# Performance work log

Measured on AMD Instinct MI355X. Metric: run time of the kernel, lower is better.

Reference implementation:

```python
import jax, jax.numpy as jnp
import numpy as np

B, S, D, H = 2, 2048, 1024, 16
DK = D // H

def setup_inputs() -> dict:
    key = jax.random.key(0)
    ks = jax.random.split(key, 11)
    scale = 1.0 / np.sqrt(D)
    inp = {
        'q': jax.random.normal(ks[0], (B, S, D), jnp.float32),
        'k': jax.random.normal(ks[1], (B, S, D), jnp.float32),
        'v': jax.random.normal(ks[2], (B, S, D), jnp.float32),
        'Wq': jax.random.normal(ks[3], (D, D), jnp.float32) * scale,
        'bq': jnp.zeros((D,), jnp.float32),
        'Wk': jax.random.normal(ks[4], (D, D), jnp.float32) * scale,
        'bk': jnp.zeros((D,), jnp.float32),
        'Wv': jax.random.normal(ks[5], (D, D), jnp.float32) * scale,
        'bv': jnp.zeros((D,), jnp.float32),
        'Wo': jax.random.normal(ks[6], (D, D), jnp.float32) * scale,
        'bo': jnp.zeros((D,), jnp.float32),
    }
    return inp

def reference(q, k, v, Wq, bq, Wk, bk, Wv, bv, Wo, bo):
    # linear projections
    qp = q @ Wq + bq   # [B,S,D]
    kp = k @ Wk + bk
    vp = v @ Wv + bv
    # split heads -> [B,H,S,DK]
    qh = qp.reshape(B, S, H, DK).transpose(0, 2, 1, 3)
    kh = kp.reshape(B, S, H, DK).transpose(0, 2, 1, 3)
    vh = vp.reshape(B, S, H, DK).transpose(0, 2, 1, 3)
    scaled = jnp.einsum('bhqd,bhkd->bhqk', qh, kh) / jnp.sqrt(jnp.float32(DK))
    attn_score = jax.nn.softmax(scaled, axis=-1)  # [B,H,S,S]
    x = jnp.einsum('bhqk,bhkd->bhqd', attn_score, vh)
    # dropout is identity in eval mode
    out = x.transpose(0, 2, 1, 3).reshape(B, S, D)
    return (out @ Wo + bo, attn_score)
```

## Files before the change

### kernel.cpp

```cpp
#include <hip/hip_runtime.h>
#include <hip/hip_bf16.h>
#include <stdint.h>
#include <stddef.h>

typedef unsigned short u16;
typedef __attribute__((ext_vector_type(8))) short short8;
typedef __attribute__((ext_vector_type(4))) short bfx4;
typedef __attribute__((ext_vector_type(4))) float f32x4;
typedef __attribute__((ext_vector_type(4))) float f4;

constexpr int B_ = 2, S_ = 2048, D_ = 1024, H_ = 16;
constexpr size_t OUT_ELEMS = (size_t)B_ * S_ * D_;

__device__ __forceinline__ u16 f2bf(float f) {
    union { float f; unsigned u; } v; v.f = f;
    unsigned r = 0x7FFFu + ((v.u >> 16) & 1u);
    return (u16)((v.u + r) >> 16);
}

__device__ __forceinline__ void gload16(const void* g, void* l) {
    auto gg = reinterpret_cast<const __attribute__((address_space(1))) unsigned*>(
        reinterpret_cast<uintptr_t>(g));
    auto ll = reinterpret_cast<__attribute__((address_space(3))) unsigned*>(
        reinterpret_cast<uintptr_t>(l));
    __builtin_amdgcn_global_load_lds(gg, ll, 16, 0, 0);
}

__global__ __launch_bounds__(256) void wtrans_kernel(
    const float* __restrict__ W0, const float* __restrict__ W1,
    const float* __restrict__ W2, const float* __restrict__ W3,
    u16* __restrict__ T0, u16* __restrict__ T1, u16* __restrict__ T2, u16* __restrict__ T3)
{
    __shared__ __align__(16) u16 Ts[64][72];
    const float* W = blockIdx.z == 0 ? W0 : blockIdx.z == 1 ? W1 : blockIdx.z == 2 ? W2 : W3;
    u16*         T = blockIdx.z == 0 ? T0 : blockIdx.z == 1 ? T1 : blockIdx.z == 2 ? T2 : T3;
    const int t = threadIdx.x;
    const int r0 = blockIdx.y * 64, c0 = blockIdx.x * 64;
    const int row = t >> 2, qd = t & 3;

    const float* src = W + (size_t)(r0 + row) * 1024 + c0 + qd * 16;
    u16 tmp[16];
    #pragma unroll
    for (int j = 0; j < 16; j += 4) {
        f4 v = *(const f4*)(src + j);
        tmp[j] = f2bf(v[0]); tmp[j+1] = f2bf(v[1]); tmp[j+2] = f2bf(v[2]); tmp[j+3] = f2bf(v[3]);
    }
    #pragma unroll
    for (int j = 0; j < 16; j++) Ts[row][qd * 16 + j] = tmp[j];
    __syncthreads();
    short8 o0, o1;
    #pragma unroll
    for (int j = 0; j < 8; j++) { o0[j] = (short)Ts[qd*16 + j][row]; o1[j] = (short)Ts[qd*16 + 8 + j][row]; }
    u16* dst = T + (size_t)(c0 + row) * 1024 + r0 + qd * 16;
    *(short8*)dst = o0;
    *(short8*)(dst + 8) = o1;
}

__global__ __launch_bounds__(256) void vtrans_kernel(const u16* __restrict__ vp, u16* __restrict__ vt)
{
    __shared__ __align__(16) u16 Vs[64][72];
    const int t = threadIdx.x;
    const int s0 = blockIdx.x * 64;
    const int bh = blockIdx.y, b = bh >> 4, h = bh & 15;
    #pragma unroll
    for (int i = 0; i < 2; i++) {
        int c = t + 256 * i, row = c >> 3, ch = c & 7;
        *(short8*)(&Vs[row][ch * 8]) =
            *(const short8*)(vp + ((size_t)b * S_ + s0 + row) * D_ + h * 64 + ch * 8);
    }
    __syncthreads();
    #pragma unroll
    for (int i = 0; i < 2; i++) {
        int c = t + 256 * i, d = c >> 3, ch = c & 7;
        short8 o;
        #pragma unroll
        for (int j = 0; j < 8; j++) o[j] = (short)Vs[ch * 8 + j][d];
        *(short8*)(vt + ((size_t)bh * 64 + d) * S_ + s0 + ch * 8) = o;
    }
}

struct Stage { short8 h[2]; };

__device__ __forceinline__ void stage_load_f32(Stage& st, const float* Af, int row0, int K, int k0, int t) {
    const int row = t >> 1, half = t & 1;
    const float* p = Af + (size_t)(row0 + row) * K + k0 + half * 16;
    #pragma unroll
    for (int j = 0; j < 2; j++) {
        f4 v0 = *(const f4*)(p + j * 8);
        f4 v1 = *(const f4*)(p + j * 8 + 4);
        short8 hh;
        hh[0]=(short)f2bf(v0[0]); hh[1]=(short)f2bf(v0[1]); hh[2]=(short)f2bf(v0[2]); hh[3]=(short)f2bf(v0[3]);
        hh[4]=(short)f2bf(v1[0]); hh[5]=(short)f2bf(v1[1]); hh[6]=(short)f2bf(v1[2]); hh[7]=(short)f2bf(v1[3]);
        st.h[j] = hh;
    }
}

__device__ __forceinline__ void stage_store_f32(const Stage& st, u16* Ls, int t) {
    const int row = t >> 1, half = t & 1;
    #pragma unroll
    for (int j = 0; j < 2; j++) {
        int byteo = half * 32 + j * 16;
        *(short8*)((char*)Ls + row * 64 + (byteo ^ ((row & 3) << 4))) = st.h[j];
    }
}

template<int A_IS_F32, int OUT_IS_F32>
__global__ __launch_bounds__(256, 3)
void gemm_bt(const void* __restrict__ A0, const void* __restrict__ A1, const void* __restrict__ A2,
             const u16* __restrict__ Bt0, const u16* __restrict__ Bt1, const u16* __restrict__ Bt2,
             const float* __restrict__ bi0, const float* __restrict__ bi1, const float* __restrict__ bi2,
             void* __restrict__ C0, void* __restrict__ C1, void* __restrict__ C2,
             int M, int N, int K, float sc0, float sc1, float sc2)
{
    __shared__ __align__(16) u16 As[2][128 * 32];
    __shared__ __align__(16) u16 Bs[2][128 * 32];

    const int z = blockIdx.z;
    const void*  Aptr  = z == 0 ? A0  : z == 1 ? A1  : A2;
    const u16*   Bt    = z == 0 ? Bt0 : z == 1 ? Bt1 : Bt2;
    const float* bias  = z == 0 ? bi0 : z == 1 ? bi1 : bi2;
    void*        Cptr  = z == 0 ? C0  : z == 1 ? C1  : C2;
    const float  scale = z == 0 ? sc0 : z == 1 ? sc1 : sc2;

    const int t = threadIdx.x;
    const int w = t >> 6, l = t & 63, lr = l >> 4, lc = l & 15;
    const int wr = w >> 1, wc = w & 1;
    const int row0 = blockIdx.y * 128, col0 = blockIdx.x * 128;
    const int NI = K >> 5;

    auto issueT = [&](const u16* P, int r0_, int i, u16* dst) {
        #pragma unroll
        for (int j = 0; j < 2; j++) {
            int off = j * 256 + t;
            int row = off >> 2, ch = off & 3;
            const char* src = (const char*)P + (((size_t)(r0_ + row) * K + i * 32) << 1)
                              + ((ch ^ (row & 3)) << 4);
            gload16(src, (char*)dst + off * 16);
        }
    };

    f32x4 acc[4][4] = {};
    Stage sa;
    issueT(Bt, col0, 0, Bs[0]);
    if constexpr (A_IS_F32) {
        stage_load_f32(sa, (const float*)Aptr, row0, K, 0, t);
        stage_store_f32(sa, As[0], t);
        stage_load_f32(sa, (const float*)Aptr, row0, K, 32, t);
    } else {
        issueT((const u16*)Aptr, row0, 0, As[0]);
    }
    __syncthreads();

    for (int i = 0; i < NI; i++) {
        const int p = i & 1;
        if (i + 1 < NI) {
            issueT(Bt, col0, i + 1, Bs[p ^ 1]);
            if constexpr (A_IS_F32) {
                stage_store_f32(sa, As[p ^ 1], t);
                const int kn = (i + 2 < NI) ? (i + 2) * 32 : 0;
                stage_load_f32(sa, (const float*)Aptr, row0, K, kn, t);
            } else {
                issueT((const u16*)Aptr, row0, i + 1, As[p ^ 1]);
            }
        }

        short8 af[4], bf_[4];
        #pragma unroll
        for (int mm = 0; mm < 4; mm++) {
            int r = wr * 64 + mm * 16 + lc;
            af[mm] = *(const short8*)((const char*)As[p] + r * 64 + ((lr * 16) ^ ((r & 3) << 4)));
        }
        #pragma unroll
        for (int nn = 0; nn < 4; nn++) {
            int r = wc * 64 + nn * 16 + lc;
            bf_[nn] = *(const short8*)((const char*)Bs[p] + r * 64 + ((lr * 16) ^ ((r & 3) << 4)));
        }
        #pragma unroll
        for (int mm = 0; mm < 4; mm++)
            #pragma unroll
            for (int nn = 0; nn < 4; nn++)
                acc[mm][nn] = __builtin_amdgcn_mfma_f32_16x16x32_bf16(af[mm], bf_[nn], acc[mm][nn], 0, 0, 0);
        __syncthreads();
    }

    float bv[4];
    #pragma unroll
    for (int nn = 0; nn < 4; nn++) bv[nn] = bias[col0 + wc * 64 + nn * 16 + lc];

    #pragma unroll
    for (int mm = 0; mm < 4; mm++) {
        const int row = row0 + wr * 64 + mm * 16 + lr * 4;
        #pragma unroll
        for (int nn = 0; nn < 4; nn++) {
            const int col = col0 + wc * 64 + nn * 16 + lc;
            #pragma unroll
            for (int r = 0; r < 4; r++) {
                float vv = (acc[mm][nn][r] + bv[nn]) * scale;
                if constexpr (OUT_IS_F32) ((float*)Cptr)[(size_t)(row + r) * N + col] = vv;
                else                      ((u16*) Cptr)[(size_t)(row + r) * N + col] = f2bf(vv);
            }
        }
    }
}

__global__ __launch_bounds__(256, 4)
void attn_kernel(const u16* __restrict__ qp, const u16* __restrict__ kp,
                 const u16* __restrict__ vt, float* __restrict__ Pout,
                 u16* __restrict__ xout)
{
    __shared__ __align__(16) u16 Qs[64 * 64];
    __shared__ __align__(16) u16 Ks[2][64 * 64];
    __shared__ __align__(16) u16 Vts[2][64 * 64];

    const int t = threadIdx.x;
    const int w = t >> 6, l = t & 63, lr = l >> 4, lc = l & 15;
    const int bid = blockIdx.x;
    const int s = ((bid & 7) << 7) | (bid >> 3);
    const int q0 = (s & 31) * 64;
    const int bh = s >> 5, b = bh >> 4, h = bh & 15;
    const float L2E = 1.4426950408889634f;
    constexpr int NT = S_ / 64;

    auto issueK = [&](int kt, int buf) {
        #pragma unroll
        for (int i = 0; i < 2; i++) {
            int off = i * 256 + t, row = off >> 3, ch = off & 7;
            const char* src = (const char*)kp + ((((size_t)b * S_ + kt * 64 + row) * D_ + h * 64) << 1)
                              + ((ch ^ (row & 7)) << 4);
            gload16(src, (char*)Ks[buf] + off * 16);
        }
    };
    auto issueV = [&](int kt, int buf) {
        #pragma unroll
        for (int i = 0; i < 2; i++) {
            int off = i * 256 + t, row = off >> 3, ch = off & 7;
            const char* src = (const char*)vt + ((((size_t)bh * 64 + row) * S_ + kt * 64) << 1)
                              + ((ch ^ (row & 7)) << 4);
            gload16(src, (char*)Vts[buf] + off * 16);
        }
    };

    issueK(0, 0);
    #pragma unroll
    for (int i = 0; i < 2; i++) {
        int c = t + 256 * i, row = c >> 3, ch = c & 7;
        short8 vq = *(const short8*)(qp + ((size_t)b * S_ + q0 + row) * D_ + h * 64 + ch * 8);
        *(short8*)((char*)Qs + row * 128 + ((ch * 16) ^ ((row & 7) << 4))) = vq;
    }
    __syncthreads();

    short8 qf[2];
    {
        int r = w * 16 + lc, sw = (r & 7) << 4;
        const char* qb = (const char*)Qs + r * 128;
        qf[0] = *(const short8*)(qb + ((lr * 16) ^ sw));
        qf[1] = *(const short8*)(qb + ((64 + lr * 16) ^ sw));
    }

    float sum = 0.f;
    for (int kt = 0; kt < NT; kt++) {
        const int p = kt & 1;
        if (kt + 1 < NT) issueK(kt + 1, p ^ 1);
        const char* Kb = (const char*)Ks[p];
        #pragma unroll
        for (int f = 0; f < 4; f++) {
            int r = f * 16 + lc, sw = (r & 7) << 4;
            const char* kb = Kb + r * 128;
            short8 k0 = *(const short8*)(kb + ((lr * 16) ^ sw));
            short8 k1 = *(const short8*)(kb + ((64 + lr * 16) ^ sw));
            f32x4 sacc = {};
            sacc = __builtin_amdgcn_mfma_f32_16x16x32_bf16(k0, qf[0], sacc, 0, 0, 0);
            sacc = __builtin_amdgcn_mfma_f32_16x16x32_bf16(k1, qf[1], sacc, 0, 0, 0);
            sum += exp2f(sacc[0] * L2E) + exp2f(sacc[1] * L2E)
                 + exp2f(sacc[2] * L2E) + exp2f(sacc[3] * L2E);
        }
        __syncthreads();
    }
    sum += __shfl_xor(sum, 16);
    sum += __shfl_xor(sum, 32);
    const float inv = 1.0f / sum;

    f32x4 xacc[4] = {};
    float* pbase = Pout + ((size_t)bh * S_ + q0 + w * 16 + lc) * S_ + lr * 4;

    issueK(0, 0); issueV(0, 0);
    __syncthreads();
    for (int kt = 0; kt < NT; kt++) {
        const int p = kt & 1;
        if (kt + 1 < NT) { issueK(kt + 1, p ^ 1); issueV(kt + 1, p ^ 1); }
        const char* Kb = (const char*)Ks[p];
        const char* Vb = (const char*)Vts[p];

        #pragma unroll
        for (int kk = 0; kk < 2; kk++) {
            union { unsigned u[4]; short8 s8; } pu;
            #pragma unroll
            for (int fo = 0; fo < 2; fo++) {
                const int f = kk * 2 + fo;
                int r = f * 16 + lc, sw = (r & 7) << 4;
                const char* kb = Kb + r * 128;
                short8 k0 = *(const short8*)(kb + ((lr * 16) ^ sw));
                short8 k1 = *(const short8*)(kb + ((64 + lr * 16) ^ sw));
                f32x4 sacc = {};
                sacc = __builtin_amdgcn_mfma_f32_16x16x32_bf16(k0, qf[0], sacc, 0, 0, 0);
                sacc = __builtin_amdgcn_mfma_f32_16x16x32_bf16(k1, qf[1], sacc, 0, 0, 0);
                f32x4 pv_;
                pv_[0] = exp2f(sacc[0] * L2E) * inv;
                pv_[1] = exp2f(sacc[1] * L2E) * inv;
                pv_[2] = exp2f(sacc[2] * L2E) * inv;
                pv_[3] = exp2f(sacc[3] * L2E) * inv;
                *(f32x4*)(pbase + (size_t)kt * 64 + f * 16) = pv_;
                pu.u[fo * 2 + 0] = (unsigned)f2bf(pv_[0]) | ((unsigned)f2bf(pv_[1]) << 16);
                pu.u[fo * 2 + 1] = (unsigned)f2bf(pv_[2]) | ((unsigned)f2bf(pv_[3]) << 16);
            }
            const short8 pa = pu.s8;
            #pragma unroll
            for (int n = 0; n < 4; n++) {
                int rr = n * 16 + lc, sw2 = (rr & 7) << 4;
                const char* vrow = Vb + rr * 128;
                union { bfx4 h[2]; short8 s8; } vu;
                vu.h[0] = *(const bfx4*)(vrow + ((kk * 64 + lr * 8) ^ sw2));
                vu.h[1] = *(const bfx4*)(vrow + ((kk * 64 + 32 + lr * 8) ^ sw2));
                xacc[n] = __builtin_amdgcn_mfma_f32_16x16x32_bf16(pa, vu.s8, xacc[n], 0, 0, 0);
            }
        }
        __syncthreads();
    }

    #pragma unroll
    for (int n = 0; n < 4; n++) {
        #pragma unroll
        for (int r = 0; r < 4; r++) {
            int row = q0 + w * 16 + lr * 4 + r;
            int col = h * 64 + n * 16 + lc;
            xout[((size_t)b * S_ + row) * D_ + col] = f2bf(xacc[n][r]);
        }
    }
}

extern "C" void kernel_launch(void* const* d_in, const int* in_sizes, int n_in,
                              void* d_out, int out_size, void* d_ws, size_t ws_size,
                              hipStream_t stream)
{
    const float* qin = (const float*)d_in[0];
    const float* kin = (const float*)d_in[1];
    const float* vin = (const float*)d_in[2];
    const float* Wq  = (const float*)d_in[3];
    const float* bq  = (const float*)d_in[4];
    const float* Wk  = (const float*)d_in[5];
    const float* bk  = (const float*)d_in[6];
    const float* Wv  = (const float*)d_in[7];
    const float* bv  = (const float*)d_in[8];
    const float* Wo  = (const float*)d_in[9];
    const float* bo  = (const float*)d_in[10];

    u16* base = (u16*)d_ws;
    u16* Wqt = base;
    u16* Wkt = base + 1048576;
    u16* Wvt = base + 2097152;
    u16* Wot = base + 3145728;
    u16* qpb = base + 4194304;
    u16* kpb = base + 8388608;
    u16* vpb = base + 12582912;
    u16* vtb = base + 16777216;
    u16* xb  = base + 20971520;

    float* out  = (float*)d_out;
    float* Pout = out + OUT_ELEMS;

    const int M = B_ * S_;

    wtrans_kernel<<<dim3(16, 16, 4), 256, 0, stream>>>(Wq, Wk, Wv, Wo, Wqt, Wkt, Wvt, Wot);
    gemm_bt<1, 0><<<dim3(8, 32, 3), 256, 0, stream>>>(
        qin, kin, vin, Wqt, Wkt, Wvt, bq, bk, bv, qpb, kpb, vpb, M, D_, D_, 0.125f, 1.0f, 1.0f);
    vtrans_kernel<<<dim3(32, 32), 256, 0, stream>>>(vpb, vtb);
    attn_kernel<<<1024, 256, 0, stream>>>(qpb, kpb, vtb, Pout, xb);
    gemm_bt<0, 1><<<dim3(8, 32, 1), 256, 0, stream>>>(
        xb, xb, xb, Wot, Wot, Wot, bo, bo, bo, out, out, out, M, D_, D_, 1.0f, 1.0f, 1.0f);
}
```

Measured before the change: 295.9 us.

## Precast inputs to bf16, remap GEMM tiles by XCD, drop LDS in attention

```diff
diff --git a/kernel.cpp b/kernel.cpp
--- a/kernel.cpp
+++ b/kernel.cpp
@@ -26,6 +26,21 @@
     __builtin_amdgcn_global_load_lds(gg, ll, 16, 0, 0);
 }
 
+__global__ __launch_bounds__(256) void cast_kernel(
+    const float* __restrict__ q, const float* __restrict__ k, const float* __restrict__ v,
+    u16* __restrict__ qo, u16* __restrict__ ko, u16* __restrict__ vo)
+{
+    const float* src = blockIdx.z == 0 ? q : blockIdx.z == 1 ? k : v;
+    u16*         dst = blockIdx.z == 0 ? qo : blockIdx.z == 1 ? ko : vo;
+    size_t i = ((size_t)blockIdx.x * 256 + threadIdx.x) * 8;
+    f4 a = *(const f4*)(src + i);
+    f4 b = *(const f4*)(src + i + 4);
+    short8 o;
+    o[0]=(short)f2bf(a[0]); o[1]=(short)f2bf(a[1]); o[2]=(short)f2bf(a[2]); o[3]=(short)f2bf(a[3]);
+    o[4]=(short)f2bf(b[0]); o[5]=(short)f2bf(b[1]); o[6]=(short)f2bf(b[2]); o[7]=(short)f2bf(b[3]);
+    *(short8*)(dst + i) = o;
+}
+
 __global__ __launch_bounds__(256) void wtrans_kernel(
     const float* __restrict__ W0, const float* __restrict__ W1,
     const float* __restrict__ W2, const float* __restrict__ W3,
@@ -79,34 +94,9 @@
     }
 }
 
-struct Stage { short8 h[2]; };
-
-__device__ __forceinline__ void stage_load_f32(Stage& st, const float* Af, int row0, int K, int k0, int t) {
-    const int row = t >> 1, half = t & 1;
-    const float* p = Af + (size_t)(row0 + row) * K + k0 + half * 16;
-    #pragma unroll
-    for (int j = 0; j < 2; j++) {
-        f4 v0 = *(const f4*)(p + j * 8);
-        f4 v1 = *(const f4*)(p + j * 8 + 4);
-        short8 hh;
-        hh[0]=(short)f2bf(v0[0]); hh[1]=(short)f2bf(v0[1]); hh[2]=(short)f2bf(v0[2]); hh[3]=(short)f2bf(v0[3]);
-        hh[4]=(short)f2bf(v1[0]); hh[5]=(short)f2bf(v1[1]); hh[6]=(short)f2bf(v1[2]); hh[7]=(short)f2bf(v1[3]);
-        st.h[j] = hh;
-    }
-}
-
-__device__ __forceinline__ void stage_store_f32(const Stage& st, u16* Ls, int t) {
-    const int row = t >> 1, half = t & 1;
-    #pragma unroll
-    for (int j = 0; j < 2; j++) {
-        int byteo = half * 32 + j * 16;
-        *(short8*)((char*)Ls + row * 64 + (byteo ^ ((row & 3) << 4))) = st.h[j];
-    }
-}
-
-template<int A_IS_F32, int OUT_IS_F32>
+template<int OUT_IS_F32>
 __global__ __launch_bounds__(256, 3)
-void gemm_bt(const void* __restrict__ A0, const void* __restrict__ A1, const void* __restrict__ A2,
+void gemm_bt(const u16* __restrict__ A0, const u16* __restrict__ A1, const u16* __restrict__ A2,
              const u16* __restrict__ Bt0, const u16* __restrict__ Bt1, const u16* __restrict__ Bt2,
              const float* __restrict__ bi0, const float* __restrict__ bi1, const float* __restrict__ bi2,
              void* __restrict__ C0, void* __restrict__ C1, void* __restrict__ C2,
@@ -116,7 +106,7 @@
     __shared__ __align__(16) u16 Bs[2][128 * 32];
 
     const int z = blockIdx.z;
-    const void*  Aptr  = z == 0 ? A0  : z == 1 ? A1  : A2;
+    const u16*   Aptr  = z == 0 ? A0  : z == 1 ? A1  : A2;
     const u16*   Bt    = z == 0 ? Bt0 : z == 1 ? Bt1 : Bt2;
     const float* bias  = z == 0 ? bi0 : z == 1 ? bi1 : bi2;
     void*        Cptr  = z == 0 ? C0  : z == 1 ? C1  : C2;
@@ -125,7 +115,10 @@
     const int t = threadIdx.x;
     const int w = t >> 6, l = t & 63, lr = l >> 4, lc = l & 15;
     const int wr = w >> 1, wc = w & 1;
-    const int row0 = blockIdx.y * 128, col0 = blockIdx.x * 128;
+    const int id = blockIdx.y * 8 + blockIdx.x;
+    const int xcd = id & 7, i_ = id >> 3;
+    const int row0 = ((xcd << 2) | ((i_ >> 4) << 1) | ((i_ >> 3) & 1)) * 128;
+    const int col0 = (i_ & 7) * 128;
     const int NI = K >> 5;
 
     auto issueT = [&](const u16* P, int r0_, int i, u16* dst) {
@@ -140,28 +133,15 @@
     };
 
     f32x4 acc[4][4] = {};
-    Stage sa;
     issueT(Bt, col0, 0, Bs[0]);
-    if constexpr (A_IS_F32) {
-        stage_load_f32(sa, (const float*)Aptr, row0, K, 0, t);
-        stage_store_f32(sa, As[0], t);
-        stage_load_f32(sa, (const float*)Aptr, row0, K, 32, t);
-    } else {
-        issueT((const u16*)Aptr, row0, 0, As[0]);
-    }
+    issueT(Aptr, row0, 0, As[0]);
     __syncthreads();
 
     for (int i = 0; i < NI; i++) {
         const int p = i & 1;
         if (i + 1 < NI) {
             issueT(Bt, col0, i + 1, Bs[p ^ 1]);
-            if constexpr (A_IS_F32) {
-                stage_store_f32(sa, As[p ^ 1], t);
-                const int kn = (i + 2 < NI) ? (i + 2) * 32 : 0;
-                stage_load_f32(sa, (const float*)Aptr, row0, K, kn, t);
-            } else {
-                issueT((const u16*)Aptr, row0, i + 1, As[p ^ 1]);
-            }
+            issueT(Aptr, row0, i + 1, As[p ^ 1]);
         }
 
         short8 af[4], bf_[4];
@@ -208,10 +188,6 @@
                  const u16* __restrict__ vt, float* __restrict__ Pout,
                  u16* __restrict__ xout)
 {
-    __shared__ __align__(16) u16 Qs[64 * 64];
-    __shared__ __align__(16) u16 Ks[2][64 * 64];
-    __shared__ __align__(16) u16 Vts[2][64 * 64];
-
     const int t = threadIdx.x;
     const int w = t >> 6, l = t & 63, lr = l >> 4, lc = l & 15;
     const int bid = blockIdx.x;
@@ -219,62 +195,25 @@
     const int q0 = (s & 31) * 64;
     const int bh = s >> 5, b = bh >> 4, h = bh & 15;
     const float L2E = 1.4426950408889634f;
-    constexpr int NT = S_ / 64;
-
-    auto issueK = [&](int kt, int buf) {
-        #pragma unroll
-        for (int i = 0; i < 2; i++) {
-            int off = i * 256 + t, row = off >> 3, ch = off & 7;
-            const char* src = (const char*)kp + ((((size_t)b * S_ + kt * 64 + row) * D_ + h * 64) << 1)
-                              + ((ch ^ (row & 7)) << 4);
-            gload16(src, (char*)Ks[buf] + off * 16);
-        }
-    };
-    auto issueV = [&](int kt, int buf) {
-        #pragma unroll
-        for (int i = 0; i < 2; i++) {
-            int off = i * 256 + t, row = off >> 3, ch = off & 7;
-            const char* src = (const char*)vt + ((((size_t)bh * 64 + row) * S_ + kt * 64) << 1)
-                              + ((ch ^ (row & 7)) << 4);
-            gload16(src, (char*)Vts[buf] + off * 16);
-        }
-    };
-
-    issueK(0, 0);
-    #pragma unroll
-    for (int i = 0; i < 2; i++) {
-        int c = t + 256 * i, row = c >> 3, ch = c & 7;
-        short8 vq = *(const short8*)(qp + ((size_t)b * S_ + q0 + row) * D_ + h * 64 + ch * 8);
-        *(short8*)((char*)Qs + row * 128 + ((ch * 16) ^ ((row & 7) << 4))) = vq;
-    }
-    __syncthreads();
-
-    short8 qf[2];
-    {
-        int r = w * 16 + lc, sw = (r & 7) << 4;
-        const char* qb = (const char*)Qs + r * 128;
-        qf[0] = *(const short8*)(qb + ((lr * 16) ^ sw));
-        qf[1] = *(const short8*)(qb + ((64 + lr * 16) ^ sw));
-    }
+
+    const u16* qrow = qp + ((size_t)b * S_ + q0 + w * 16 + lc) * D_ + h * 64;
+    const short8 qf0 = *(const short8*)(qrow + lr * 8);
+    const short8 qf1 = *(const short8*)(qrow + 32 + lr * 8);
+
+    const u16* kbase = kp + (size_t)b * S_ * D_ + h * 64;
+    const u16* vbase = vt + (size_t)bh * 64 * S_;
 
     float sum = 0.f;
-    for (int kt = 0; kt < NT; kt++) {
-        const int p = kt & 1;
-        if (kt + 1 < NT) issueK(kt + 1, p ^ 1);
-        const char* Kb = (const char*)Ks[p];
-        #pragma unroll
-        for (int f = 0; f < 4; f++) {
-            int r = f * 16 + lc, sw = (r & 7) << 4;
-            const char* kb = Kb + r * 128;
-            short8 k0 = *(const short8*)(kb + ((lr * 16) ^ sw));
-            short8 k1 = *(const short8*)(kb + ((64 + lr * 16) ^ sw));
-            f32x4 sacc = {};
-            sacc = __builtin_amdgcn_mfma_f32_16x16x32_bf16(k0, qf[0], sacc, 0, 0, 0);
-            sacc = __builtin_amdgcn_mfma_f32_16x16x32_bf16(k1, qf[1], sacc, 0, 0, 0);
-            sum += exp2f(sacc[0] * L2E) + exp2f(sacc[1] * L2E)
-                 + exp2f(sacc[2] * L2E) + exp2f(sacc[3] * L2E);
-        }
-        __syncthreads();
+    #pragma unroll 2
+    for (int kg = 0; kg < S_ / 16; kg++) {
+        const u16* krow = kbase + (size_t)(kg * 16 + lc) * D_;
+        short8 k0 = *(const short8*)(krow + lr * 8);
+        short8 k1 = *(const short8*)(krow + 32 + lr * 8);
+        f32x4 sacc = {};
+        sacc = __builtin_amdgcn_mfma_f32_16x16x32_bf16(k0, qf0, sacc, 0, 0, 0);
+        sacc = __builtin_amdgcn_mfma_f32_16x16x32_bf16(k1, qf1, sacc, 0, 0, 0);
+        sum += exp2f(sacc[0] * L2E) + exp2f(sacc[1] * L2E)
+             + exp2f(sacc[2] * L2E) + exp2f(sacc[3] * L2E);
     }
     sum += __shfl_xor(sum, 16);
     sum += __shfl_xor(sum, 32);
@@ -283,48 +222,33 @@
     f32x4 xacc[4] = {};
     float* pbase = Pout + ((size_t)bh * S_ + q0 + w * 16 + lc) * S_ + lr * 4;
 
-    issueK(0, 0); issueV(0, 0);
-    __syncthreads();
-    for (int kt = 0; kt < NT; kt++) {
-        const int p = kt & 1;
-        if (kt + 1 < NT) { issueK(kt + 1, p ^ 1); issueV(kt + 1, p ^ 1); }
-        const char* Kb = (const char*)Ks[p];
-        const char* Vb = (const char*)Vts[p];
-
-        #pragma unroll
-        for (int kk = 0; kk < 2; kk++) {
-            union { unsigned u[4]; short8 s8; } pu;
-            #pragma unroll
-            for (int fo = 0; fo < 2; fo++) {
-                const int f = kk * 2 + fo;
-                int r = f * 16 + lc, sw = (r & 7) << 4;
-                const char* kb = Kb + r * 128;
-                short8 k0 = *(const short8*)(kb + ((lr * 16) ^ sw));
-                short8 k1 = *(const short8*)(kb + ((64 + lr * 16) ^ sw));
-                f32x4 sacc = {};
-                sacc = __builtin_amdgcn_mfma_f32_16x16x32_bf16(k0, qf[0], sacc, 0, 0, 0);
-                sacc = __builtin_amdgcn_mfma_f32_16x16x32_bf16(k1, qf[1], sacc, 0, 0, 0);
-                f32x4 pv_;
-                pv_[0] = exp2f(sacc[0] * L2E) * inv;
-                pv_[1] = exp2f(sacc[1] * L2E) * inv;
-                pv_[2] = exp2f(sacc[2] * L2E) * inv;
-                pv_[3] = exp2f(sacc[3] * L2E) * inv;
-                *(f32x4*)(pbase + (size_t)kt * 64 + f * 16) = pv_;
-                pu.u[fo * 2 + 0] = (unsigned)f2bf(pv_[0]) | ((unsigned)f2bf(pv_[1]) << 16);
-                pu.u[fo * 2 + 1] = (unsigned)f2bf(pv_[2]) | ((unsigned)f2bf(pv_[3]) << 16);
-            }
-            const short8 pa = pu.s8;
-            #pragma unroll
-            for (int n = 0; n < 4; n++) {
-                int rr = n * 16 + lc, sw2 = (rr & 7) << 4;
-                const char* vrow = Vb + rr * 128;
-                union { bfx4 h[2]; short8 s8; } vu;
-                vu.h[0] = *(const bfx4*)(vrow + ((kk * 64 + lr * 8) ^ sw2));
-                vu.h[1] = *(const bfx4*)(vrow + ((kk * 64 + 32 + lr * 8) ^ sw2));
-                xacc[n] = __builtin_amdgcn_mfma_f32_16x16x32_bf16(pa, vu.s8, xacc[n], 0, 0, 0);
-            }
-        }
-        __syncthreads();
+    for (int kc = 0; kc < S_ / 32; kc++) {
+        union { unsigned u[4]; short8 s8; } pu;
+        #pragma unroll
+        for (int fo = 0; fo < 2; fo++) {
+            const u16* krow = kbase + (size_t)(kc * 32 + fo * 16 + lc) * D_;
+            short8 k0 = *(const short8*)(krow + lr * 8);
+            short8 k1 = *(const short8*)(krow + 32 + lr * 8);
+            f32x4 sacc = {};
+            sacc = __builtin_amdgcn_mfma_f32_16x16x32_bf16(k0, qf0, sacc, 0, 0, 0);
+            sacc = __builtin_amdgcn_mfma_f32_16x16x32_bf16(k1, qf1, sacc, 0, 0, 0);
+            f32x4 pv_;
+            pv_[0] = exp2f(sacc[0] * L2E) * inv;
+            pv_[1] = exp2f(sacc[1] * L2E) * inv;
+            pv_[2] = exp2f(sacc[2] * L2E) * inv;
+            pv_[3] = exp2f(sacc[3] * L2E) * inv;
+            __builtin_nontemporal_store(pv_, (f32x4*)(pbase + kc * 32 + fo * 16));
+            pu.u[fo * 2 + 0] = (unsigned)f2bf(pv_[0]) | ((unsigned)f2bf(pv_[1]) << 16);
+            pu.u[fo * 2 + 1] = (unsigned)f2bf(pv_[2]) | ((unsigned)f2bf(pv_[3]) << 16);
+        }
+        #pragma unroll
+        for (int n = 0; n < 4; n++) {
+            const u16* vrow = vbase + (size_t)(n * 16 + lc) * S_ + kc * 32;
+            union { bfx4 h[2]; short8 s8; } vu;
+            vu.h[0] = *(const bfx4*)(vrow + lr * 4);
+            vu.h[1] = *(const bfx4*)(vrow + 16 + lr * 4);
+            xacc[n] = __builtin_amdgcn_mfma_f32_16x16x32_bf16(pu.s8, vu.s8, xacc[n], 0, 0, 0);
+        }
     }
 
     #pragma unroll
@@ -364,6 +288,9 @@
     u16* vpb = base + 12582912;
     u16* vtb = base + 16777216;
     u16* xb  = base + 20971520;
+    u16* qcb = base + 25165824;
+    u16* kcb = base + 29360128;
+    u16* vcb = base + 33554432;
 
     float* out  = (float*)d_out;
     float* Pout = out + OUT_ELEMS;
@@ -371,10 +298,11 @@
     const int M = B_ * S_;
 
     wtrans_kernel<<<dim3(16, 16, 4), 256, 0, stream>>>(Wq, Wk, Wv, Wo, Wqt, Wkt, Wvt, Wot);
-    gemm_bt<1, 0><<<dim3(8, 32, 3), 256, 0, stream>>>(
-        qin, kin, vin, Wqt, Wkt, Wvt, bq, bk, bv, qpb, kpb, vpb, M, D_, D_, 0.125f, 1.0f, 1.0f);
+    cast_kernel<<<dim3(2048, 1, 3), 256, 0, stream>>>(qin, kin, vin, qcb, kcb, vcb);
+    gemm_bt<0><<<dim3(8, 32, 3), 256, 0, stream>>>(
+        qcb, kcb, vcb, Wqt, Wkt, Wvt, bq, bk, bv, qpb, kpb, vpb, M, D_, D_, 0.125f, 1.0f, 1.0f);
     vtrans_kernel<<<dim3(32, 32), 256, 0, stream>>>(vpb, vtb);
     attn_kernel<<<1024, 256, 0, stream>>>(qpb, kpb, vtb, Pout, xb);
-    gemm_bt<0, 1><<<dim3(8, 32, 1), 256, 0, stream>>>(
+    gemm_bt<1><<<dim3(8, 32, 1), 256, 0, stream>>>(
         xb, xb, xb, Wot, Wot, Wot, bo, bo, bo, out, out, out, M, D_, D_, 1.0f, 1.0f, 1.0f);
 }
```

New measurement: 540.8 us. 1.83x slower.
